# Performance work log

Measured on AMD Instinct MI355X. Metric: run time of the kernel, lower is better.

## Reference

```python
import jax, jax.numpy as jnp
import numpy as np

NUM_HEADS = 16
TOP_K = 2
ROPE_BASE = 10000.0
LN_EPS = 1e-5


def _rope_sin_cos(S, D, dtype):
    # D = head_dim; inv_freq over even indices, shape [D//2]
    inv_freq = 1.0 / (ROPE_BASE ** (jnp.arange(0, D, 2, dtype=jnp.float32) / D))
    freqs = jnp.arange(S, dtype=jnp.float32)[:, None] * inv_freq[None, :]  # [S, D//2]
    sin = jnp.sin(freqs).astype(dtype)[None, :, None, :]  # [1,S,1,D//2]
    cos = jnp.cos(freqs).astype(dtype)[None, :, None, :]
    return sin, cos


def _apply_rope(x, sin, cos):
    # x: [B,S,H,D]; rotate interleaved even/odd pairs
    x1, x2 = x[..., 0::2], x[..., 1::2]
    r1 = x1 * cos - x2 * sin
    r2 = x1 * sin + x2 * cos
    return jnp.stack([r1, r2], axis=-1).reshape(x.shape)


def _layer_norm(x, w, b):
    mu = jnp.mean(x, axis=-1, keepdims=True)
    var = jnp.mean(jnp.square(x - mu), axis=-1, keepdims=True)
    return (x - mu) * jax.lax.rsqrt(var + LN_EPS) * w + b


def reference(x, in_proj_w, in_proj_b, out_proj_w, out_proj_b,
              gate_w, gate_b, expert_w, expert_b,
              ln1_w, ln1_b, ln2_w, ln2_b):
    B, S, E = x.shape
    H = NUM_HEADS
    D = E // H

    # --- RoPE on q and k (per-head) ---
    xh = x.reshape(B, S, H, D)
    sin, cos = _rope_sin_cos(S, D, x.dtype)
    q_in = _apply_rope(xh, sin, cos).reshape(B, S, E)
    k_in = q_in  # q = k in the module
    v_in = x

    # --- MultiheadAttention (eval, causal mask) ---
    Wq, Wk, Wv = jnp.split(in_proj_w, 3, axis=0)  # each [E,E]
    bq, bk, bv = jnp.split(in_proj_b, 3, axis=0)
    q = (q_in @ Wq.T + bq).reshape(B, S, H, D)
    k = (k_in @ Wk.T + bk).reshape(B, S, H, D)
    v = (v_in @ Wv.T + bv).reshape(B, S, H, D)

    scale = 1.0 / jnp.sqrt(jnp.asarray(D, dtype=x.dtype))
    scores = jnp.einsum('bqhd,bkhd->bhqk', q, k) * scale  # [B,H,S,S]
    causal = jnp.tril(jnp.ones((S, S), dtype=bool))
    scores = jnp.where(causal[None, None], scores, jnp.asarray(-jnp.inf, dtype=scores.dtype))
    attn = jax.nn.softmax(scores, axis=-1)
    ctx = jnp.einsum('bhqk,bkhd->bqhd', attn, v).reshape(B, S, E)
    attn_out = ctx @ out_proj_w.T + out_proj_b

    x1 = _layer_norm(x + attn_out, ln1_w, ln1_b)

    # --- MoE: dense all-experts compute + top-k gather/combine ---
    gates = jax.nn.softmax(x1 @ gate_w.T + gate_b, axis=-1)  # [B,S,Eexp]
    _, top_idx = jax.lax.top_k(gates, TOP_K)                 # [B,S,K]
    top_gates = jnp.take_along_axis(gates, top_idx, axis=-1)  # differentiable gather
    # expert_outputs: [B,S,Eexp,E]
    expert_outputs = jnp.einsum('bsd,efd->bsef', x1, expert_w) + expert_b[None, None]
    sel = jnp.take_along_axis(
        expert_outputs, top_idx[..., None], axis=2)  # [B,S,K,E]
    moe_out = jnp.sum(sel * top_gates[..., None], axis=2)    # [B,S,E]

    return _layer_norm(x1 + moe_out, ln2_w, ln2_b)


def setup_inputs() -> dict:
    key = jax.random.key(0)
    ks = jax.random.split(key, 8)
    B, S, E, NE = 2, 2048, 1024, 8
    s = 0.02
    return {
        'x': jax.random.normal(ks[0], (B, S, E), dtype=jnp.float32),
        'in_proj_w': jax.random.normal(ks[1], (3 * E, E), dtype=jnp.float32) * s,
        'in_proj_b': jnp.zeros((3 * E,), dtype=jnp.float32),
        'out_proj_w': jax.random.normal(ks[2], (E, E), dtype=jnp.float32) * s,
        'out_proj_b': jnp.zeros((E,), dtype=jnp.float32),
        'gate_w': jax.random.normal(ks[3], (NE, E), dtype=jnp.float32) * s,
        'gate_b': jnp.zeros((NE,), dtype=jnp.float32),
        'expert_w': jax.random.normal(ks[4], (NE, E, E), dtype=jnp.float32) * s,
        'expert_b': jnp.zeros((NE, E), dtype=jnp.float32),
        'ln1_w': jnp.ones((E,), dtype=jnp.float32),
        'ln1_b': jnp.zeros((E,), dtype=jnp.float32),
        'ln2_w': jnp.ones((E,), dtype=jnp.float32),
        'ln2_b': jnp.zeros((E,), dtype=jnp.float32),
    }
```

## Files before the change

### kernel.cpp

```cpp
#include <hip/hip_runtime.h>
#include <hip/hip_bf16.h>
#include <stdint.h>

#define B_  2
#define S_  2048
#define E_  1024
#define H_  16
#define D_  64
#define NE_ 8
#define M_  4096

typedef unsigned short u16;
typedef _Float16 f16x8 __attribute__((ext_vector_type(8)));
typedef float f32x4 __attribute__((ext_vector_type(4)));

__device__ __forceinline__ f32x4 fzero4() { f32x4 v; v[0]=0.f; v[1]=0.f; v[2]=0.f; v[3]=0.f; return v; }

__device__ __forceinline__ u16 hbits(_Float16 h) { union { _Float16 f; u16 u; } c; c.f = h; return c.u; }
__device__ __forceinline__ u16 f2h(float v) { return hbits((_Float16)v); }

__device__ __forceinline__ void storeA3(u16* p, size_t stride, float v) {
  _Float16 h = (_Float16)v; float hf = (float)h;
  p[0]        = hbits(h);
  p[stride]   = f2h(hf * 0.015625f);
  p[2*stride] = f2h((v - hf) * 64.0f);
}
__device__ __forceinline__ void storeW3(u16* p, size_t stride, float v) {
  _Float16 h = (_Float16)v; float hf = (float)h;
  p[0]        = hbits(h);
  p[stride]   = f2h((v - hf) * 64.0f);
  p[2*stride] = f2h(hf * 0.015625f);
}
__device__ __forceinline__ void store2s(u16* p, size_t stride, float v) {
  _Float16 h = (_Float16)v; float hf = (float)h;
  p[0]      = hbits(h);
  p[stride] = f2h((v - hf) * 64.0f);
}

__device__ __forceinline__ void gload_lds16(const void* g, void* l) {
  __builtin_amdgcn_global_load_lds(
      (const __attribute__((address_space(1))) void*)g,
      (__attribute__((address_space(3))) void*)l, 16, 0, 0);
}

#define MFMA16(a, b, c) __builtin_amdgcn_mfma_f32_16x16x32_f16((a), (b), (c), 0, 0, 0)

__global__ __launch_bounds__(256) void k_splitW(const float* __restrict__ in, u16* __restrict__ out, int total) {
  int idx = blockIdx.x * 256 + threadIdx.x;
  if (idx >= total) return;
  int n = idx >> 10, k = idx & 1023;
  storeW3(out + (size_t)n * 3072 + k, 1024, in[idx]);
}

__global__ __launch_bounds__(256) void k_convH(const float* __restrict__ in, u16* __restrict__ out, int total) {
  int idx = blockIdx.x * 256 + threadIdx.x;
  if (idx < total) out[idx] = f2h(in[idx]);
}

__global__ __launch_bounds__(256) void k_rope3(const float* __restrict__ x, u16* __restrict__ ropeA, u16* __restrict__ xA) {
  int p = blockIdx.x * 256 + threadIdx.x;
  if (p >= B_ * S_ * H_ * 32) return;
  int i   = p & 31;
  int h   = (p >> 5) & 15;
  int row = p >> 9;
  int s   = row & (S_ - 1);
  int col = h * 64 + 2 * i;
  size_t base = (size_t)row * E_ + col;
  float x1 = x[base], x2 = x[base + 1];
  float inv = exp2f(-(float)i * 0.41524101186092029f);
  float ang = (float)s * inv;
  float sn, cs; sincosf(ang, &sn, &cs);
  float r1 = x1 * cs - x2 * sn;
  float r2 = x1 * sn + x2 * cs;
  size_t ob = (size_t)row * 3072 + col;
  storeA3(ropeA + ob,     1024, r1);
  storeA3(ropeA + ob + 1, 1024, r2);
  storeA3(xA + ob,        1024, x1);
  storeA3(xA + ob + 1,    1024, x2);
}

__global__ __launch_bounds__(256) void gemm_qkv(
    const u16* __restrict__ ropeA, const u16* __restrict__ xA,
    const u16* __restrict__ Wall, const float* __restrict__ ipb,
    u16* __restrict__ q2, u16* __restrict__ k2, u16* __restrict__ vt2)
{
  __shared__ __align__(16) u16 lA[128 * 32];
  __shared__ __align__(16) u16 lB[128 * 32];
  const int tid  = threadIdx.x;
  const int lane = tid & 63;
  const int wid  = tid >> 6;
  const int nt = blockIdx.x, mt = blockIdx.y;
  const u16* A = (nt < 16) ? ropeA : xA;
  long aoff[2], boff[2];
#pragma unroll
  for (int i = 0; i < 2; ++i) {
    aoff[i] = (long)(mt * 128 + i * 64 + (tid >> 2)) * 3072 + (tid & 3) * 8;
    boff[i] = (long)(nt * 128 + i * 64 + (tid >> 2)) * 3072 + (tid & 3) * 8;
  }
  f32x4 acc[4][4];
#pragma unroll
  for (int a = 0; a < 4; ++a)
#pragma unroll
    for (int b = 0; b < 4; ++b) acc[a][b] = fzero4();
  const int wm = wid >> 1, wn = wid & 1;
  const int r16 = lane & 15, g4 = lane >> 4;

  for (int k0 = 0; k0 < 3072; k0 += 32) {
#pragma unroll
    for (int i = 0; i < 2; ++i) {
      gload_lds16(A    + aoff[i] + k0, (char*)lA + i * 4096 + wid * 1024);
      gload_lds16(Wall + boff[i] + k0, (char*)lB + i * 4096 + wid * 1024);
    }
    __syncthreads();
    f16x8 af[4], bf[4];
#pragma unroll
    for (int f = 0; f < 4; ++f) {
      af[f] = *(const f16x8*)&lA[(wm * 64 + f * 16 + r16) * 32 + 8 * g4];
      bf[f] = *(const f16x8*)&lB[(wn * 64 + f * 16 + r16) * 32 + 8 * g4];
    }
#pragma unroll
    for (int fm = 0; fm < 4; ++fm)
#pragma unroll
      for (int fn = 0; fn < 4; ++fn)
        acc[fm][fn] = MFMA16(af[fm], bf[fn], acc[fm][fn]);
    __syncthreads();
  }

  const int m0 = mt * 128 + wm * 64;
  const int n0 = nt * 128 + wn * 64;
  const size_t PLV = (size_t)B_ * H_ * 64 * S_;
#pragma unroll
  for (int fm = 0; fm < 4; ++fm) {
#pragma unroll
    for (int fn = 0; fn < 4; ++fn) {
      const int colg = n0 + fn * 16 + r16;
      const float bv = ipb[colg];
#pragma unroll
      for (int i = 0; i < 4; ++i) {
        const int rowg = m0 + fm * 16 + 4 * g4 + i;
        float v = acc[fm][fn][i] + bv;
        int bb = rowg >> 11, s = rowg & 2047;
        if (nt < 16) {
          int col = colg & 1023, hh = col >> 6, d = col & 63;
          u16* tgt = (colg < 1024) ? q2 : k2;
          store2s(tgt + (((size_t)(bb * H_ + hh)) * S_ + s) * 128 + d, 64, v);
        } else {
          int col = colg - 2048, hh = col >> 6, d = col & 63;
          store2s(vt2 + (((size_t)(bb * H_ + hh)) * 64 + d) * (size_t)S_ + s, PLV, v);
        }
      }
    }
  }
}

template <int EPI, bool GATHER, int BN>
__global__ __launch_bounds__(256) void gemm_bt(
    const u16* __restrict__ A, const u16* __restrict__ Bw,
    const float* __restrict__ bias, void* __restrict__ Cout,
    int M, int N, int K,
    const int* __restrict__ lists, const int* __restrict__ cnt,
    const float* __restrict__ topw)
{
  constexpr int BCH = BN / 64;
  constexpr int FN  = BN / 32;
  __shared__ __align__(16) u16 lA[128 * 32];
  __shared__ __align__(16) u16 lB[BN * 32];
  const int tid  = threadIdx.x;
  const int lane = tid & 63;
  const int wid  = tid >> 6;
  const int nt = blockIdx.x, mt = blockIdx.y;
  int cnt_e = 0;
  const int* listE = nullptr;
  if constexpr (GATHER) {
    int e = blockIdx.z;
    cnt_e = cnt[e];
    if (mt * 128 >= cnt_e) return;
    Bw   += (size_t)e * N * K;
    bias += (size_t)e * N;
    listE = lists + e * 4096;
  }
  long aoff[2], boff[BCH];
#pragma unroll
  for (int i = 0; i < 2; ++i) {
    long arow;
    if constexpr (GATHER) {
      int li = mt * 128 + i * 64 + (tid >> 2);
      int entry = (li < cnt_e) ? listE[li] : 0;
      arow = entry >> 1;
    } else {
      arow = mt * 128 + i * 64 + (tid >> 2);
    }
    aoff[i] = arow * (long)K + (tid & 3) * 8;
  }
#pragma unroll
  for (int i = 0; i < BCH; ++i)
    boff[i] = (long)(nt * BN + i * 64 + (tid >> 2)) * K + (tid & 3) * 8;

  f32x4 acc[4][FN];
#pragma unroll
  for (int a = 0; a < 4; ++a)
#pragma unroll
    for (int b = 0; b < FN; ++b) acc[a][b] = fzero4();
  const int wm = wid >> 1, wn = wid & 1;
  const int r16 = lane & 15, g4 = lane >> 4;

  for (int k0 = 0; k0 < K; k0 += 32) {
#pragma unroll
    for (int i = 0; i < 2; ++i)
      gload_lds16(A + aoff[i] + k0, (char*)lA + i * 4096 + wid * 1024);
#pragma unroll
    for (int i = 0; i < BCH; ++i)
      gload_lds16(Bw + boff[i] + k0, (char*)lB + i * 4096 + wid * 1024);
    __syncthreads();
    f16x8 af[4], bf[FN];
#pragma unroll
    for (int f = 0; f < 4; ++f)
      af[f] = *(const f16x8*)&lA[(wm * 64 + f * 16 + r16) * 32 + 8 * g4];
#pragma unroll
    for (int f = 0; f < FN; ++f)
      bf[f] = *(const f16x8*)&lB[(wn * (FN * 16) + f * 16 + r16) * 32 + 8 * g4];
#pragma unroll
    for (int fm = 0; fm < 4; ++fm)
#pragma unroll
      for (int fn = 0; fn < FN; ++fn)
        acc[fm][fn] = MFMA16(af[fm], bf[fn], acc[fm][fn]);
    __syncthreads();
  }

  const int m0 = mt * 128 + wm * 64;
  const int n0 = nt * BN + wn * (FN * 16);
#pragma unroll
  for (int fm = 0; fm < 4; ++fm) {
#pragma unroll
    for (int fn = 0; fn < FN; ++fn) {
      const int colg = n0 + fn * 16 + r16;
      const float bv = bias[colg];
#pragma unroll
      for (int i = 0; i < 4; ++i) {
        const int rowg = m0 + fm * 16 + 4 * g4 + i;
        float v = acc[fm][fn][i] + bv;
        if constexpr (EPI == 2) {
          ((float*)Cout)[(size_t)rowg * N + colg] = v;
        } else {
          if (rowg < cnt_e) {
            int entry = listE[rowg];
            ((float*)Cout)[(size_t)entry * 1024 + colg] = v * topw[entry];
          }
        }
      }
    }
  }
}

__global__ __launch_bounds__(256) void k_attn4(const u16* __restrict__ Q2, const u16* __restrict__ K2,
                                               const u16* __restrict__ VT2, u16* __restrict__ ctx3) {
  __shared__ __align__(16) u16 Kl[2][64 * 128];
  __shared__ __align__(16) u16 Vl[2][2 * 64 * 64];
  __shared__ __align__(16) u16 Pl[4][2 * 1024];
  const int tid  = threadIdx.x;
  const int w    = tid >> 6;
  const int lane = tid & 63;
  const int r16 = lane & 15, g4 = lane >> 4;

  const int bid  = blockIdx.x;
  const int xcd  = bid & 7;
  const int slot = bid >> 3;
  const int rnd  = slot >> 5;
  const int c    = slot & 31;
  const int bh   = xcd + 8 * rnd;
  const int cc   = (rnd >= 2) ? ((c + 8) & 31) : c;
  const int qb   = (rnd & 1) ? cc : (31 - cc);
  const int nkt  = qb + 1;

  const size_t PLV = (size_t)B_ * H_ * 64 * S_;
  const u16* Qp = Q2  + (size_t)bh * S_ * 128;
  const u16* Kp = K2  + (size_t)bh * S_ * 128;
  const u16* Vp = VT2 + (size_t)bh * 64 * S_;
  const int qw0 = qb * 64 + w * 16;

  f16x8 qh[2], ql[2];
#pragma unroll
  for (int t = 0; t < 2; ++t) {
    qh[t] = *(const f16x8*)&Qp[(size_t)(qw0 + r16) * 128 + t * 32 + 8 * g4];
    ql[t] = *(const f16x8*)&Qp[(size_t)(qw0 + r16) * 128 + 64 + t * 32 + 8 * g4];
  }

  float mrow[4], lrow[4];
  f32x4 om[4], ox[4];
#pragma unroll
  for (int i = 0; i < 4; ++i) { mrow[i] = -1e30f; lrow[i] = 0.f; }
#pragma unroll
  for (int db = 0; db < 4; ++db) { om[db] = fzero4(); ox[db] = fzero4(); }

  auto STAGE = [&](int buf, int k0) {
#pragma unroll
    for (int c4 = 0; c4 < 4; ++c4) {
      const int li = c4 * 4 + w;
      {
        const int row = li * 4 + (lane >> 4);
        const int so  = ((lane & 15) ^ (row & 7)) * 8;
        gload_lds16(Kp + (size_t)(k0 + row) * 128 + so,
                    (char*)&Kl[buf][0] + li * 1024);
      }
      {
        const int plane = li >> 3;
        const int d     = (li & 7) * 8 + (lane >> 3);
        const int so    = ((lane & 7) ^ (d & 7)) * 8;
        gload_lds16(Vp + (size_t)plane * PLV + (size_t)d * S_ + k0 + so,
                    (char*)&Vl[buf][0] + li * 1024);
      }
    }
  };

  STAGE(0, 0);
  __syncthreads();

  for (int kt = 0; kt < nkt; ++kt) {
    const int buf = kt & 1;
    const int k0  = kt * 64;
    if (kt + 1 < nkt) STAGE(buf ^ 1, k0 + 64);

    f32x4 sm[4], sx[4];
#pragma unroll
    for (int ks = 0; ks < 4; ++ks) { sm[ks] = fzero4(); sx[ks] = fzero4(); }
#pragma unroll
    for (int ks = 0; ks < 4; ++ks) {
      const int row = ks * 16 + r16;
#pragma unroll
      for (int t = 0; t < 2; ++t) {
        const int sw = ((t * 4 + g4) ^ (r16 & 7)) * 8;
        f16x8 kh = *(const f16x8*)&Kl[buf][row * 128 + sw];
        f16x8 kl = *(const f16x8*)&Kl[buf][row * 128 + 64 + sw];
        sm[ks] = MFMA16(qh[t], kh, sm[ks]);
        sx[ks] = MFMA16(qh[t], kl, sx[ks]);
        sx[ks] = MFMA16(ql[t], kh, sx[ks]);
      }
    }

    float pv[4][4], corr[4];
#pragma unroll
    for (int i = 0; i < 4; ++i) {
      const int qg = qw0 + 4 * g4 + i;
      float s[4];
      float mx = -1e30f;
#pragma unroll
      for (int ks = 0; ks < 4; ++ks) {
        float v = (sm[ks][i] + sx[ks][i] * 0.015625f) * 0.125f;
        if (k0 + ks * 16 + r16 > qg) v = -1e30f;
        s[ks] = v;
        mx = fmaxf(mx, v);
      }
      mx = fmaxf(mx, __shfl_xor(mx, 1));
      mx = fmaxf(mx, __shfl_xor(mx, 2));
      mx = fmaxf(mx, __shfl_xor(mx, 4));
      mx = fmaxf(mx, __shfl_xor(mx, 8));
      float mn = fmaxf(mrow[i], mx);
      float cr = __expf(mrow[i] - mn);
      float rs = 0.f;
#pragma unroll
      for (int ks = 0; ks < 4; ++ks) {
        float e = __expf(s[ks] - mn);
        pv[ks][i] = e;
        rs += e;
      }
      rs += __shfl_xor(rs, 1);
      rs += __shfl_xor(rs, 2);
      rs += __shfl_xor(rs, 4);
      rs += __shfl_xor(rs, 8);
      lrow[i] = lrow[i] * cr + rs;
      mrow[i] = mn;
      corr[i] = cr;
    }
#pragma unroll
    for (int db = 0; db < 4; ++db)
#pragma unroll
      for (int i = 0; i < 4; ++i) { om[db][i] *= corr[i]; ox[db][i] *= corr[i]; }

#pragma unroll
    for (int ks = 0; ks < 4; ++ks) {
      const int sl = ks * 2 + (r16 >> 3);
#pragma unroll
      for (int i = 0; i < 4; ++i) {
        const int pr = 4 * g4 + i;
        const int ad = pr * 64 + ((sl ^ (pr & 7)) * 8) + (r16 & 7);
        float p = pv[ks][i];
        _Float16 h = (_Float16)p; float hf = (float)h;
        Pl[w][ad]        = hbits(h);
        Pl[w][1024 + ad] = f2h((p - hf) * 64.0f);
      }
    }
    asm volatile("s_waitcnt lgkmcnt(0)" ::: "memory");
    __builtin_amdgcn_sched_barrier(0);

#pragma unroll
    for (int kk = 0; kk < 2; ++kk) {
      const int psw = ((kk * 4 + g4) ^ (r16 & 7)) * 8;
      f16x8 ph  = *(const f16x8*)&Pl[w][r16 * 64 + psw];
      f16x8 pl2 = *(const f16x8*)&Pl[w][1024 + r16 * 64 + psw];
#pragma unroll
      for (int db = 0; db < 4; ++db) {
        const int d = db * 16 + r16;
        const int vsw = ((kk * 4 + g4) ^ (r16 & 7)) * 8;
        f16x8 vh  = *(const f16x8*)&Vl[buf][d * 64 + vsw];
        f16x8 vl2 = *(const f16x8*)&Vl[buf][4096 + d * 64 + vsw];
        om[db] = MFMA16(ph, vh, om[db]);
        ox[db] = MFMA16(ph, vl2, ox[db]);
        ox[db] = MFMA16(pl2, vh, ox[db]);
      }
    }
    __syncthreads();
  }

  const int b = bh >> 4, h = bh & 15;
#pragma unroll
  for (int db = 0; db < 4; ++db) {
#pragma unroll
    for (int i = 0; i < 4; ++i) {
      const int srow = qw0 + 4 * g4 + i;
      float val = (om[db][i] + ox[db][i] * 0.015625f) / lrow[i];
      size_t rb = ((size_t)(b * S_ + srow)) * 3072 + h * 64 + db * 16 + r16;
      storeA3(ctx3 + rb, 1024, val);
    }
  }
}

__device__ __forceinline__ float block_sum256(float v, float* red) {
#pragma unroll
  for (int off = 32; off > 0; off >>= 1) v += __shfl_down(v, off);
  const int wid = threadIdx.x >> 6;
  if ((threadIdx.x & 63) == 0) red[wid] = v;
  __syncthreads();
  float tot = red[0] + red[1] + red[2] + red[3];
  __syncthreads();
  return tot;
}

__global__ __launch_bounds__(256) void k_ln1(const float* __restrict__ x, const float* __restrict__ ao,
                                             const float* __restrict__ w, const float* __restrict__ bb,
                                             float* __restrict__ x1f, u16* __restrict__ x1h) {
  const int row = blockIdx.x, t = threadIdx.x;
  __shared__ float red[4];
  f32x4 xv = ((const f32x4*)(x  + (size_t)row * 1024))[t];
  f32x4 av = ((const f32x4*)(ao + (size_t)row * 1024))[t];
  f32x4 v  = xv + av;
  float tot = block_sum256(v[0] + v[1] + v[2] + v[3], red);
  float mu = tot * (1.0f / 1024.0f);
  f32x4 d = v - mu;
  float totq = block_sum256(d[0]*d[0] + d[1]*d[1] + d[2]*d[2] + d[3]*d[3], red);
  float rs = rsqrtf(totq * (1.0f / 1024.0f) + 1e-5f);
  f32x4 wv = ((const f32x4*)w)[t];
  f32x4 bv = ((const f32x4*)bb)[t];
  f32x4 o;
#pragma unroll
  for (int j = 0; j < 4; ++j) o[j] = d[j] * rs * wv[j] + bv[j];
  ((f32x4*)(x1f + (size_t)row * 1024))[t] = o;
#pragma unroll
  for (int j = 0; j < 4; ++j) x1h[(size_t)row * 1024 + t * 4 + j] = f2h(o[j]);
}

__global__ __launch_bounds__(256) void k_ln2(const float* __restrict__ x1f, const float* __restrict__ pair,
                                             const float* __restrict__ w, const float* __restrict__ bb,
                                             float* __restrict__ out) {
  const int row = blockIdx.x, t = threadIdx.x;
  __shared__ float red[4];
  f32x4 v  = ((const f32x4*)(x1f + (size_t)row * 1024))[t];
  f32x4 pa = ((const f32x4*)(pair + ((size_t)row * 2)     * 1024))[t];
  f32x4 pb = ((const f32x4*)(pair + ((size_t)row * 2 + 1) * 1024))[t];
  v = v + pa + pb;
  float tot = block_sum256(v[0] + v[1] + v[2] + v[3], red);
  float mu = tot * (1.0f / 1024.0f);
  f32x4 d = v - mu;
  float totq = block_sum256(d[0]*d[0] + d[1]*d[1] + d[2]*d[2] + d[3]*d[3], red);
  float rs = rsqrtf(totq * (1.0f / 1024.0f) + 1e-5f);
  f32x4 wv = ((const f32x4*)w)[t];
  f32x4 bv = ((const f32x4*)bb)[t];
  f32x4 o;
#pragma unroll
  for (int j = 0; j < 4; ++j) o[j] = d[j] * rs * wv[j] + bv[j];
  ((f32x4*)out)[(size_t)row * 256 + t] = o;
}

__global__ __launch_bounds__(64) void k_zero(int* p, int n) {
  int i = threadIdx.x;
  if (i < n) p[i] = 0;
}

__global__ __launch_bounds__(64) void k_gate(const float* __restrict__ x1f,
                                             const float* __restrict__ gw, const float* __restrict__ gb,
                                             float* __restrict__ topw, int* __restrict__ cnt, int* __restrict__ lists) {
  const int t = blockIdx.x, lane = threadIdx.x;
  const f32x4* xr = (const f32x4*)(x1f + (size_t)t * 1024);
  f32x4 xv[4];
#pragma unroll
  for (int c = 0; c < 4; ++c) xv[c] = xr[lane * 4 + c];
  float logit[8];
#pragma unroll
  for (int e = 0; e < 8; ++e) {
    const f32x4* wr = (const f32x4*)(gw + (size_t)e * 1024);
    float a = 0.f;
#pragma unroll
    for (int c = 0; c < 4; ++c) {
      f32x4 wv = wr[lane * 4 + c];
      a += xv[c][0]*wv[0] + xv[c][1]*wv[1] + xv[c][2]*wv[2] + xv[c][3]*wv[3];
    }
#pragma unroll
    for (int off = 32; off > 0; off >>= 1) a += __shfl_xor(a, off);
    logit[e] = a + gb[e];
  }
  if (lane == 0) {
    float mx = logit[0];
#pragma unroll
    for (int e = 1; e < 8; ++e) mx = fmaxf(mx, logit[e]);
    float g[8], se = 0.f;
#pragma unroll
    for (int e = 0; e < 8; ++e) { g[e] = __expf(logit[e] - mx); se += g[e]; }
    float inv = 1.0f / se;
#pragma unroll
    for (int e = 0; e < 8; ++e) g[e] *= inv;
    int e1 = 0;
#pragma unroll
    for (int e = 1; e < 8; ++e) if (g[e] > g[e1]) e1 = e;
    int e2 = (e1 == 0) ? 1 : 0;
#pragma unroll
    for (int e = 0; e < 8; ++e) if (e != e1 && g[e] > g[e2]) e2 = e;
    topw[t * 2]     = g[e1];
    topw[t * 2 + 1] = g[e2];
    int p1 = atomicAdd(&cnt[e1], 1); lists[e1 * 4096 + p1] = t * 2;
    int p2 = atomicAdd(&cnt[e2], 1); lists[e2 * 4096 + p2] = t * 2 + 1;
  }
}

extern "C" void kernel_launch(void* const* d_in, const int* in_sizes, int n_in,
                              void* d_out, int out_size, void* d_ws, size_t ws_size,
                              hipStream_t stream) {
  const float* x    = (const float*)d_in[0];
  const float* ipw  = (const float*)d_in[1];
  const float* ipb  = (const float*)d_in[2];
  const float* opw  = (const float*)d_in[3];
  const float* opb  = (const float*)d_in[4];
  const float* gw   = (const float*)d_in[5];
  const float* gb   = (const float*)d_in[6];
  const float* ew   = (const float*)d_in[7];
  const float* eb   = (const float*)d_in[8];
  const float* ln1w = (const float*)d_in[9];
  const float* ln1b = (const float*)d_in[10];
  const float* ln2w = (const float*)d_in[11];
  const float* ln2b = (const float*)d_in[12];
  char* ws = (char*)d_ws;

  constexpr size_t OF_WQKV = 0;
  constexpr size_t OF_WOUT = OF_WQKV + (size_t)3072*3072*2;
  constexpr size_t OF_WEXP = OF_WOUT + (size_t)1024*3072*2;
  constexpr size_t OF_RA   = OF_WEXP + (size_t)8*1024*1024*2;
  constexpr size_t OF_RB   = OF_RA + (size_t)4096*3072*2;
  constexpr size_t OF_RC   = OF_RB + (size_t)4096*3072*2;
  constexpr size_t OF_RD   = OF_RC + (size_t)16777216;
  constexpr size_t OF_RE   = OF_RD + (size_t)16777216;
  constexpr size_t OF_TOPW = OF_RE + (size_t)16777216;
  constexpr size_t OF_CNT  = OF_TOPW + 32768;
  constexpr size_t OF_LIST = OF_CNT + 256;

  u16*   Wqkv3 = (u16*)(ws + OF_WQKV);
  u16*   Wout3 = (u16*)(ws + OF_WOUT);
  u16*   WexpH = (u16*)(ws + OF_WEXP);
  u16*   rope3 = (u16*)(ws + OF_RA);
  u16*   ctx3  = (u16*)(ws + OF_RA);
  u16*   x3    = (u16*)(ws + OF_RB);
  float* attn  = (float*)(ws + OF_RB);
  u16*   x1h   = (u16*)(ws + OF_RB + (size_t)16777216);
  u16*   q2    = (u16*)(ws + OF_RC);
  float* x1f   = (float*)(ws + OF_RC);
  u16*   k2    = (u16*)(ws + OF_RD);
  u16*   vt2   = (u16*)(ws + OF_RE);
  float* pair  = (float*)(ws + OF_RD);
  float* topw  = (float*)(ws + OF_TOPW);
  int*   cnt   = (int*)(ws + OF_CNT);
  int*   lists = (int*)(ws + OF_LIST);

  (void)in_sizes; (void)n_in; (void)out_size; (void)ws_size;

  k_splitW<<<dim3((3072*1024)/256), 256, 0, stream>>>(ipw, Wqkv3, 3072*1024);
  k_splitW<<<dim3((1024*1024)/256), 256, 0, stream>>>(opw, Wout3, 1024*1024);
  k_convH <<<dim3((8*1024*1024)/256), 256, 0, stream>>>(ew, WexpH, 8*1024*1024);
  k_rope3 <<<dim3(2097152/256), 256, 0, stream>>>(x, rope3, x3);

  gemm_qkv<<<dim3(24, 32), 256, 0, stream>>>(rope3, x3, Wqkv3, ipb, q2, k2, vt2);

  k_attn4<<<dim3(1024), 256, 0, stream>>>(q2, k2, vt2, ctx3);

  gemm_bt<2,false,64><<<dim3(16,32), 256, 0, stream>>>(ctx3, Wout3, opb, attn, M_, 1024, 3072, nullptr, nullptr, nullptr);

  k_ln1<<<dim3(M_), 256, 0, stream>>>(x, attn, ln1w, ln1b, x1f, x1h);

  k_zero<<<1, 64, 0, stream>>>(cnt, 8);
  k_gate<<<dim3(M_), 64, 0, stream>>>(x1f, gw, gb, topw, cnt, lists);

  gemm_bt<3,true,64><<<dim3(16,32,8), 256, 0, stream>>>(x1h, WexpH, eb, pair, M_, 1024, 1024, lists, cnt, topw);

  k_ln2<<<dim3(M_), 256, 0, stream>>>(x1f, pair, ln2w, ln2b, (float*)d_out);
}
```

Measured before the change: 651.6 us.

## Process two query tiles per attention block to reuse staged K/V tiles

The flash-attention kernel now handles 128 query rows per workgroup (two 64-row groups per wave set) instead of 64, so each K/V tile loaded into LDS feeds twice the MFMA work. The grid halves to 512 blocks and the causal work-balancing map is redone for 16 query blocks per head. Fully masked tiles of the first group skip softmax and PV. The cost is roughly doubled accumulator and Q register use, which may lower occupancy, plus fewer blocks to spread across CUs.

After: 704.8 us. 1.08x slower.

```diff
diff --git a/kernel.cpp b/kernel.cpp
--- a/kernel.cpp
+++ b/kernel.cpp
@@ -252,7 +252,7 @@
   }
 }
 
-__global__ __launch_bounds__(256) void k_attn4(const u16* __restrict__ Q2, const u16* __restrict__ K2,
+__global__ __launch_bounds__(256) void k_attn8(const u16* __restrict__ Q2, const u16* __restrict__ K2,
                                                const u16* __restrict__ VT2, u16* __restrict__ ctx3) {
   __shared__ __align__(16) u16 Kl[2][64 * 128];
   __shared__ __align__(16) u16 Vl[2][2 * 64 * 64];
@@ -265,32 +265,40 @@
   const int bid  = blockIdx.x;
   const int xcd  = bid & 7;
   const int slot = bid >> 3;
-  const int rnd  = slot >> 5;
-  const int c    = slot & 31;
+  const int rnd  = slot >> 4;
+  const int c    = slot & 15;
   const int bh   = xcd + 8 * rnd;
-  const int cc   = (rnd >= 2) ? ((c + 8) & 31) : c;
-  const int qb   = (rnd & 1) ? cc : (31 - cc);
-  const int nkt  = qb + 1;
+  const int qb   = (rnd == 0 || rnd == 3) ? (15 - c) : c;
+  const int nkt  = 2 * qb + 2;
 
   const size_t PLV = (size_t)B_ * H_ * 64 * S_;
   const u16* Qp = Q2  + (size_t)bh * S_ * 128;
   const u16* Kp = K2  + (size_t)bh * S_ * 128;
   const u16* Vp = VT2 + (size_t)bh * 64 * S_;
-  const int qw0 = qb * 64 + w * 16;
-
-  f16x8 qh[2], ql[2];
-#pragma unroll
-  for (int t = 0; t < 2; ++t) {
-    qh[t] = *(const f16x8*)&Qp[(size_t)(qw0 + r16) * 128 + t * 32 + 8 * g4];
-    ql[t] = *(const f16x8*)&Qp[(size_t)(qw0 + r16) * 128 + 64 + t * 32 + 8 * g4];
-  }
-
-  float mrow[4], lrow[4];
-  f32x4 om[4], ox[4];
-#pragma unroll
-  for (int i = 0; i < 4; ++i) { mrow[i] = -1e30f; lrow[i] = 0.f; }
-#pragma unroll
-  for (int db = 0; db < 4; ++db) { om[db] = fzero4(); ox[db] = fzero4(); }
+  const int qrow0 = qb * 128 + w * 16;
+  const int qrow1 = qrow0 + 64;
+
+  f16x8 qh[2][2], ql[2][2];
+#pragma unroll
+  for (int g = 0; g < 2; ++g) {
+    const int qr = qrow0 + g * 64;
+#pragma unroll
+    for (int t = 0; t < 2; ++t) {
+      qh[g][t] = *(const f16x8*)&Qp[(size_t)(qr + r16) * 128 + t * 32 + 8 * g4];
+      ql[g][t] = *(const f16x8*)&Qp[(size_t)(qr + r16) * 128 + 64 + t * 32 + 8 * g4];
+    }
+  }
+
+  float mrow[2][4], lrow[2][4];
+  f32x4 om[2][4], ox[2][4];
+#pragma unroll
+  for (int g = 0; g < 2; ++g)
+#pragma unroll
+    for (int i = 0; i < 4; ++i) { mrow[g][i] = -1e30f; lrow[g][i] = 0.f; }
+#pragma unroll
+  for (int g = 0; g < 2; ++g)
+#pragma unroll
+    for (int db = 0; db < 4; ++db) { om[g][db] = fzero4(); ox[g][db] = fzero4(); }
 
   auto STAGE = [&](int buf, int k0) {
 #pragma unroll
@@ -320,9 +328,11 @@
     const int k0  = kt * 64;
     if (kt + 1 < nkt) STAGE(buf ^ 1, k0 + 64);
 
-    f32x4 sm[4], sx[4];
-#pragma unroll
-    for (int ks = 0; ks < 4; ++ks) { sm[ks] = fzero4(); sx[ks] = fzero4(); }
+    f32x4 sm[2][4], sx[2][4];
+#pragma unroll
+    for (int g = 0; g < 2; ++g)
+#pragma unroll
+      for (int ks = 0; ks < 4; ++ks) { sm[g][ks] = fzero4(); sx[g][ks] = fzero4(); }
 #pragma unroll
     for (int ks = 0; ks < 4; ++ks) {
       const int row = ks * 16 + r16;
@@ -331,95 +341,109 @@
         const int sw = ((t * 4 + g4) ^ (r16 & 7)) * 8;
         f16x8 kh = *(const f16x8*)&Kl[buf][row * 128 + sw];
         f16x8 kl = *(const f16x8*)&Kl[buf][row * 128 + 64 + sw];
-        sm[ks] = MFMA16(qh[t], kh, sm[ks]);
-        sx[ks] = MFMA16(qh[t], kl, sx[ks]);
-        sx[ks] = MFMA16(ql[t], kh, sx[ks]);
-      }
-    }
-
-    float pv[4][4], corr[4];
-#pragma unroll
-    for (int i = 0; i < 4; ++i) {
-      const int qg = qw0 + 4 * g4 + i;
-      float s[4];
-      float mx = -1e30f;
+#pragma unroll
+        for (int g = 0; g < 2; ++g) {
+          sm[g][ks] = MFMA16(qh[g][t], kh, sm[g][ks]);
+          sx[g][ks] = MFMA16(qh[g][t], kl, sx[g][ks]);
+          sx[g][ks] = MFMA16(ql[g][t], kh, sx[g][ks]);
+        }
+      }
+    }
+
+#pragma unroll
+    for (int g = 0; g < 2; ++g) {
+      const int qw0 = qrow0 + g * 64;
+      if (g == 0 && k0 > qrow0 + 15) continue;
+
+      float pv[4][4], corr[4];
+#pragma unroll
+      for (int i = 0; i < 4; ++i) {
+        const int qg = qw0 + 4 * g4 + i;
+        float s[4];
+        float mx = -1e30f;
+#pragma unroll
+        for (int ks = 0; ks < 4; ++ks) {
+          float v = (sm[g][ks][i] + sx[g][ks][i] * 0.015625f) * 0.125f;
+          if (k0 + ks * 16 + r16 > qg) v = -1e30f;
+          s[ks] = v;
+          mx = fmaxf(mx, v);
+        }
+        mx = fmaxf(mx, __shfl_xor(mx, 1));
+        mx = fmaxf(mx, __shfl_xor(mx, 2));
+        mx = fmaxf(mx, __shfl_xor(mx, 4));
+        mx = fmaxf(mx, __shfl_xor(mx, 8));
+        float mn = fmaxf(mrow[g][i], mx);
+        float cr = __expf(mrow[g][i] - mn);
+        float rs = 0.f;
+#pragma unroll
+        for (int ks = 0; ks < 4; ++ks) {
+          float e = __expf(s[ks] - mn);
+          pv[ks][i] = e;
+          rs += e;
+        }
+        rs += __shfl_xor(rs, 1);
+        rs += __shfl_xor(rs, 2);
+        rs += __shfl_xor(rs, 4);
+        rs += __shfl_xor(rs, 8);
+        lrow[g][i] = lrow[g][i] * cr + rs;
+        mrow[g][i] = mn;
+        corr[i] = cr;
+      }
+#pragma unroll
+      for (int db = 0; db < 4; ++db)
+#pragma unroll
+        for (int i = 0; i < 4; ++i) { om[g][db][i] *= corr[i]; ox[g][db][i] *= corr[i]; }
+
 #pragma unroll
       for (int ks = 0; ks < 4; ++ks) {
-        float v = (sm[ks][i] + sx[ks][i] * 0.015625f) * 0.125f;
-        if (k0 + ks * 16 + r16 > qg) v = -1e30f;
-        s[ks] = v;
-        mx = fmaxf(mx, v);
-      }
-      mx = fmaxf(mx, __shfl_xor(mx, 1));
-      mx = fmaxf(mx, __shfl_xor(mx, 2));
-      mx = fmaxf(mx, __shfl_xor(mx, 4));
-      mx = fmaxf(mx, __shfl_xor(mx, 8));
-      float mn = fmaxf(mrow[i], mx);
-      float cr = __expf(mrow[i] - mn);
-      float rs = 0.f;
-#pragma unroll
-      for (int ks = 0; ks < 4; ++ks) {
-        float e = __expf(s[ks] - mn);
-        pv[ks][i] = e;
-        rs += e;
-      }
-      rs += __shfl_xor(rs, 1);
-      rs += __shfl_xor(rs, 2);
-      rs += __shfl_xor(rs, 4);
-      rs += __shfl_xor(rs, 8);
-      lrow[i] = lrow[i] * cr + rs;
-      mrow[i] = mn;
-      corr[i] = cr;
-    }
-#pragma unroll
-    for (int db = 0; db < 4; ++db)
-#pragma unroll
-      for (int i = 0; i < 4; ++i) { om[db][i] *= corr[i]; ox[db][i] *= corr[i]; }
-
-#pragma unroll
-    for (int ks = 0; ks < 4; ++ks) {
-      const int sl = ks * 2 + (r16 >> 3);
+        const int sl = ks * 2 + (r16 >> 3);
+#pragma unroll
+        for (int i = 0; i < 4; ++i) {
+          const int pr = 4 * g4 + i;
+          const int ad = pr * 64 + ((sl ^ (pr & 7)) * 8) + (r16 & 7);
+          float p = pv[ks][i];
+          _Float16 h = (_Float16)p; float hf = (float)h;
+          Pl[w][ad]        = hbits(h);
+          Pl[w][1024 + ad] = f2h((p - hf) * 64.0f);
+        }
+      }
+      asm volatile("s_waitcnt lgkmcnt(0)" ::: "memory");
+      __builtin_amdgcn_sched_barrier(0);
+
+#pragma unroll
+      for (int kk = 0; kk < 2; ++kk) {
+        const int psw = ((kk * 4 + g4) ^ (r16 & 7)) * 8;
+        f16x8 ph  = *(const f16x8*)&Pl[w][r16 * 64 + psw];
+        f16x8 pl2 = *(const f16x8*)&Pl[w][1024 + r16 * 64 + psw];
+#pragma unroll
+        for (int db = 0; db < 4; ++db) {
+          const int d = db * 16 + r16;
+          const int vsw = ((kk * 4 + g4) ^ (r16 & 7)) * 8;
+          f16x8 vh  = *(const f16x8*)&Vl[buf][d * 64 + vsw];
+          f16x8 vl2 = *(const f16x8*)&Vl[buf][4096 + d * 64 + vsw];
+          om[g][db] = MFMA16(ph, vh, om[g][db]);
+          ox[g][db] = MFMA16(ph, vl2, ox[g][db]);
+          ox[g][db] = MFMA16(pl2, vh, ox[g][db]);
+        }
+      }
+      asm volatile("s_waitcnt lgkmcnt(0)" ::: "memory");
+      __builtin_amdgcn_sched_barrier(0);
+    }
+    __syncthreads();
+  }
+
+  const int b = bh >> 4, h = bh & 15;
+#pragma unroll
+  for (int g = 0; g < 2; ++g) {
+#pragma unroll
+    for (int db = 0; db < 4; ++db) {
 #pragma unroll
       for (int i = 0; i < 4; ++i) {
-        const int pr = 4 * g4 + i;
-        const int ad = pr * 64 + ((sl ^ (pr & 7)) * 8) + (r16 & 7);
-        float p = pv[ks][i];
-        _Float16 h = (_Float16)p; float hf = (float)h;
-        Pl[w][ad]        = hbits(h);
-        Pl[w][1024 + ad] = f2h((p - hf) * 64.0f);
-      }
-    }
-    asm volatile("s_waitcnt lgkmcnt(0)" ::: "memory");
-    __builtin_amdgcn_sched_barrier(0);
-
-#pragma unroll
-    for (int kk = 0; kk < 2; ++kk) {
-      const int psw = ((kk * 4 + g4) ^ (r16 & 7)) * 8;
-      f16x8 ph  = *(const f16x8*)&Pl[w][r16 * 64 + psw];
-      f16x8 pl2 = *(const f16x8*)&Pl[w][1024 + r16 * 64 + psw];
-#pragma unroll
-      for (int db = 0; db < 4; ++db) {
-        const int d = db * 16 + r16;
-        const int vsw = ((kk * 4 + g4) ^ (r16 & 7)) * 8;
-        f16x8 vh  = *(const f16x8*)&Vl[buf][d * 64 + vsw];
-        f16x8 vl2 = *(const f16x8*)&Vl[buf][4096 + d * 64 + vsw];
-        om[db] = MFMA16(ph, vh, om[db]);
-        ox[db] = MFMA16(ph, vl2, ox[db]);
-        ox[db] = MFMA16(pl2, vh, ox[db]);
-      }
-    }
-    __syncthreads();
-  }
-
-  const int b = bh >> 4, h = bh & 15;
-#pragma unroll
-  for (int db = 0; db < 4; ++db) {
-#pragma unroll
-    for (int i = 0; i < 4; ++i) {
-      const int srow = qw0 + 4 * g4 + i;
-      float val = (om[db][i] + ox[db][i] * 0.015625f) / lrow[i];
-      size_t rb = ((size_t)(b * S_ + srow)) * 3072 + h * 64 + db * 16 + r16;
-      storeA3(ctx3 + rb, 1024, val);
+        const int srow = qrow0 + g * 64 + 4 * g4 + i;
+        float val = (om[g][db][i] + ox[g][db][i] * 0.015625f) / lrow[g][i];
+        size_t rb = ((size_t)(b * S_ + srow)) * 3072 + h * 64 + db * 16 + r16;
+        storeA3(ctx3 + rb, 1024, val);
+      }
     }
   }
 }
@@ -586,7 +610,7 @@
 
   gemm_qkv<<<dim3(24, 32), 256, 0, stream>>>(rope3, x3, Wqkv3, ipb, q2, k2, vt2);
 
-  k_attn4<<<dim3(1024), 256, 0, stream>>>(q2, k2, vt2, ctx3);
+  k_attn8<<<dim3(512), 256, 0, stream>>>(q2, k2, vt2, ctx3);
 
   gemm_bt<2,false,64><<<dim3(16,32), 256, 0, stream>>>(ctx3, Wout3, opb, attn, M_, 1024, 3072, nullptr, nullptr, nullptr);
 
```
